# Kernel tuning notes

Hardware: AMD Instinct MI355X
Metric: run time of the kernel (lower is better)

Reference implementation:

```python
import jax, jax.numpy as jnp
import numpy as np

B, N, D, H = 2, 1024, 512, 16
DH = D // H  # d_head = 32
NEG_INF = -1e9
LN_EPS = 1e-5


def setup_inputs() -> dict:
    key = jax.random.key(0)
    ks = jax.random.split(key, 12)
    x = jax.random.normal(ks[0], (B, N, D), dtype=jnp.float32)
    pdist = jax.random.uniform(ks[1], (B, N, N), dtype=jnp.float32)
    angle = jax.random.normal(ks[2], (B, N, N, 2), dtype=jnp.float32)
    adj = jax.random.uniform(ks[3], (B, N, N), dtype=jnp.float32)
    mask = jnp.zeros((B, 1, 1, N), dtype=bool)
    # parameters
    gamma_p = jnp.ones((H,), dtype=jnp.float32)
    gamma_adj = jnp.ones((H,), dtype=jnp.float32)
    w_bias = jax.random.normal(ks[4], (H, 2), dtype=jnp.float32) / np.sqrt(2.0)   # Linear(2,H).weight
    att_w = jax.random.normal(ks[5], (3 * H * DH, D), dtype=jnp.float32) / np.sqrt(D)  # Linear(D,3HDh).weight
    ff_w = jax.random.normal(ks[6], (D, H * DH), dtype=jnp.float32) / np.sqrt(H * DH)  # Linear(HDh,D).weight
    ff_b = jnp.zeros((D,), dtype=jnp.float32)
    ln_w = jnp.ones((D,), dtype=jnp.float32)
    ln_b = jnp.zeros((D,), dtype=jnp.float32)
    return dict(x=x, pdist=pdist, angle=angle, adj=adj, mask=mask,
                gamma_p=gamma_p, gamma_adj=gamma_adj, w_bias=w_bias,
                att_w=att_w, ff_w=ff_w, ff_b=ff_b, ln_w=ln_w, ln_b=ln_b)


def reference(x, pdist, angle, adj, mask, gamma_p, gamma_adj, w_bias,
              att_w, ff_w, ff_b, ln_w, ln_b):
    bsz, n_atoms, _ = x.shape
    # QKV projection
    qkv = x @ att_w.T                              # [B,N,3*H*DH]
    wq, wk, wv = jnp.split(qkv, 3, axis=-1)
    wq = wq.reshape(bsz, n_atoms, H, DH)
    wk = wk.reshape(bsz, n_atoms, H, DH)
    wv = wv.reshape(bsz, n_atoms, H, DH)
    # scores with additive biases
    score = jnp.einsum('bihd,bjhd->bhij', wq, wk) / jnp.sqrt(jnp.float32(DH))
    score = score - gamma_p[None, :, None, None] * pdist[:, None]
    angle_bias = jnp.einsum('bijc,hc->bhij', angle, w_bias)
    score = score + angle_bias
    score = score + gamma_adj[None, :, None, None] * adj[:, None]
    score = jnp.where(mask, NEG_INF, score)
    prob = jax.nn.softmax(score, axis=-1)          # [B,H,N,N]
    att_vec = jnp.einsum('bhij,bjhd->bihd', prob, wv).reshape(bsz, n_atoms, H * DH)
    ff_out = att_vec @ ff_w.T + ff_b               # [B,N,D]
    y = x + ff_out
    mu = jnp.mean(y, axis=-1, keepdims=True)
    var = jnp.mean(jnp.square(y - mu), axis=-1, keepdims=True)
    return (y - mu) / jnp.sqrt(var + LN_EPS) * ln_w + ln_b
```

## Files before the change

kernel.cpp:

```cpp
#include <hip/hip_runtime.h>
#include <hip/hip_bf16.h>
#include <stdint.h>

#define DEVI __device__ __forceinline__

typedef __attribute__((ext_vector_type(4))) float f32x4;
typedef __attribute__((ext_vector_type(16))) float f32x16;
typedef __attribute__((ext_vector_type(8))) short bf16x8;

constexpr int nB = 2, nN = 1024, nD = 512, nH = 16, nDH = 32;

DEVI unsigned short f2bf(float x) {
  unsigned u = __float_as_uint(x);
  return (unsigned short)((u + 0x7fffu + ((u >> 16) & 1u)) >> 16);
}
DEVI float bf2f(unsigned short s) { return __uint_as_float(((unsigned)s) << 16); }
DEVI unsigned pk2(float lo, float hi_) {
  return (unsigned)f2bf(lo) | ((unsigned)f2bf(hi_) << 16);
}
DEVI float bperm(int srclane, float v) {
  return __int_as_float(__builtin_amdgcn_ds_bpermute(srclane << 2, __float_as_int(v)));
}
DEVI void gload16(const void* g, void* l) {
  __builtin_amdgcn_global_load_lds((const __attribute__((address_space(1))) void*)g,
                                   (__attribute__((address_space(3))) void*)l, 16, 0, 0);
}

__global__ __launch_bounds__(256) void cvt_kernel(const float* __restrict__ x,
                                                  const float* __restrict__ aw,
                                                  const float* __restrict__ fw,
                                                  unsigned short* __restrict__ xb,
                                                  unsigned short* __restrict__ awb,
                                                  unsigned short* __restrict__ fwb) {
  int i = blockIdx.x * 256 + threadIdx.x;
  const float* src; unsigned short* dst; int base;
  if (i < 262144)      { src = x;  dst = xb;  base = i; }
  else if (i < 458752) { src = aw; dst = awb; base = i - 262144; }
  else                 { src = fw; dst = fwb; base = i - 458752; }
  float4 v = reinterpret_cast<const float4*>(src)[base];
  ushort4 o;
  o.x = f2bf(v.x); o.y = f2bf(v.y); o.z = f2bf(v.z); o.w = f2bf(v.w);
  reinterpret_cast<ushort4*>(dst)[base] = o;
}

template <int BM, int BN, int MODE>
__global__ __launch_bounds__(256) void gemm_bt(const unsigned short* __restrict__ A,
                                               const unsigned short* __restrict__ Bw,
                                               unsigned short* __restrict__ q,
                                               unsigned short* __restrict__ kmat,
                                               unsigned short* __restrict__ vm,
                                               float* __restrict__ C,
                                               int K, int Ncols) {
  constexpr int MW = BM / 2, NW = BN / 2;
  constexpr int MF = MW / 16, NF = NW / 16;
  constexpr int IA = BM / 16, IB = BN / 16, PW = (IA + IB) / 4;
  __shared__ __align__(16) unsigned short sA[BM * 32];
  __shared__ __align__(16) unsigned short sB[BN * 32];
  const int tid = threadIdx.x, wid = tid >> 6, lane = tid & 63;
  const int wr = wid >> 1, wc = wid & 1;
  const long rowA = (long)blockIdx.x * BM;
  const long rowB = (long)blockIdx.y * BN;
  const int srow = lane >> 2, scol = (lane & 3) * 8;

  f32x4 acc[MF][NF];
#pragma unroll
  for (int mm = 0; mm < MF; ++mm)
#pragma unroll
    for (int nn = 0; nn < NF; ++nn)
#pragma unroll
      for (int r = 0; r < 4; ++r) acc[mm][nn][r] = 0.f;

  for (int k0 = 0; k0 < K; k0 += 32) {
    __syncthreads();
#pragma unroll
    for (int j = 0; j < PW; ++j) {
      int g = wid + 4 * j;
      if (g < IA) {
        gload16(&A[(rowA + g * 16 + srow) * K + k0 + scol], &sA[g * 512]);
      } else {
        int c = g - IA;
        gload16(&Bw[(rowB + c * 16 + srow) * K + k0 + scol], &sB[c * 512]);
      }
    }
    __syncthreads();
    const int kg = (lane >> 4) * 8, rlo = lane & 15;
    bf16x8 af[MF], bfv[NF];
#pragma unroll
    for (int mm = 0; mm < MF; ++mm)
      af[mm] = *reinterpret_cast<const bf16x8*>(&sA[(MW * wr + 16 * mm + rlo) * 32 + kg]);
#pragma unroll
    for (int nn = 0; nn < NF; ++nn)
      bfv[nn] = *reinterpret_cast<const bf16x8*>(&sB[(NW * wc + 16 * nn + rlo) * 32 + kg]);
#pragma unroll
    for (int mm = 0; mm < MF; ++mm)
#pragma unroll
      for (int nn = 0; nn < NF; ++nn)
        acc[mm][nn] = __builtin_amdgcn_mfma_f32_16x16x32_bf16(af[mm], bfv[nn],
                                                              acc[mm][nn], 0, 0, 0);
  }

#pragma unroll
  for (int mm = 0; mm < MF; ++mm)
#pragma unroll
    for (int nn = 0; nn < NF; ++nn)
#pragma unroll
      for (int r = 0; r < 4; ++r) {
        float v = acc[mm][nn][r];
        int row = (int)rowA + MW * wr + 16 * mm + (lane >> 4) * 4 + r;
        int col = (int)rowB + NW * wc + 16 * nn + (lane & 15);
        if constexpr (MODE == 0) {
          int s = col >> 9, rem = col & 511;
          int h = rem >> 5, d = rem & 31;
          int b = row >> 10, n = row & 1023;
          long idx = ((long)(b * nH + h) * nN + n) * nDH + d;
          if (s == 0)      q[idx]    = f2bf(v * 0.1767766952966369f);
          else if (s == 1) kmat[idx] = f2bf(v);
          else             vm[idx]   = f2bf(v);
        } else {
          C[(long)row * Ncols + col] = v;
        }
      }
}

__global__ __launch_bounds__(256) void vtrans_kernel(const unsigned short* __restrict__ vm,
                                                     unsigned short* __restrict__ vtt) {
  const int g = blockIdx.x, bh = g >> 3, oct = g & 7;
  const int t = threadIdx.x;
  __shared__ unsigned short tile[32][36];
  for (int s = 0; s < 4; ++s) {
    const int jt = oct * 4 + s;
    {
      int r = t >> 3, c4 = (t & 7) * 4;
      *reinterpret_cast<ushort4*>(&tile[r][c4]) = *reinterpret_cast<const ushort4*>(
          vm + ((long)bh * nN + jt * 32 + r) * 32 + c4);
    }
    __syncthreads();
    {
      int d = t >> 3, j4 = (t & 7) * 4;
      ushort4 o;
      o.x = tile[j4][d]; o.y = tile[j4 + 1][d];
      o.z = tile[j4 + 2][d]; o.w = tile[j4 + 3][d];
      *reinterpret_cast<ushort4*>(vtt + ((long)bh * 32 + jt) * 1024 + d * 32 + j4) = o;
    }
    __syncthreads();
  }
}

__global__ __launch_bounds__(512, 4) void attn_kernel(
    const unsigned short* __restrict__ qm, const unsigned short* __restrict__ km,
    const unsigned short* __restrict__ vtt,
    const float* __restrict__ pdist, const float* __restrict__ angle,
    const float* __restrict__ adj, const unsigned char* __restrict__ mask,
    const float* __restrict__ gamma_p, const float* __restrict__ gamma_adj,
    const float* __restrict__ w_bias,
    unsigned short* __restrict__ po, float* __restrict__ pm, float* __restrict__ pl) {
  const int b = blockIdx.x >> 5, it = blockIdx.x & 31;
  const int jc = blockIdx.y, hg = blockIdx.z;
  const int tid = threadIdx.x, wid = tid >> 6, lane = tid & 63;
  const int h = hg * 8 + wid;
  const int li = lane & 31, hi = lane >> 5;
  const int ibase = it * 32;

  __shared__ __align__(16) float s_pd[32 * 32], s_adj[32 * 32];
  __shared__ __align__(16) float s_a0[32 * 32], s_a1[32 * 32];
  __shared__ __align__(16) float s_mkf[32];

  const float gp = gamma_p[h], ga = gamma_adj[h];
  const float wb0 = w_bias[2 * h], wb1 = w_bias[2 * h + 1];

  const unsigned short* qb = qm + ((long)(b * nH + h) * nN + ibase) * nDH;
  const bf16x8 qf0 = *reinterpret_cast<const bf16x8*>(qb + li * 32 + hi * 8);
  const bf16x8 qf1 = *reinterpret_cast<const bf16x8*>(qb + li * 32 + 16 + hi * 8);

  f32x16 o;
#pragma unroll
  for (int r = 0; r < 16; ++r) o[r] = 0.f;
  float mrun = -INFINITY, lrun = 0.f;

  for (int s = 0; s < 8; ++s) {
    const int jt = jc * 8 + s, jbase = jt * 32;
    __syncthreads();
    {
      int r = (tid >> 3) & 31, c = tid & 7;
      const float* src = (tid < 256 ? pdist : adj) +
                         ((long)b * nN + ibase + r) * nN + jbase + c * 4;
      float4 v = *reinterpret_cast<const float4*>(src);
      float* dst = (tid < 256 ? s_pd : s_adj) + r * 32 + ((c ^ (r & 7)) << 2);
      *reinterpret_cast<float4*>(dst) = v;
    }
    {
      int r = tid >> 4, p = tid & 15;
      float4 v = *reinterpret_cast<const float4*>(
          angle + (((long)b * nN + ibase + r) * nN + jbase + p * 2) * 2);
      int off = r * 32 + (((p >> 1) ^ (r & 7)) << 2) + (p & 1) * 2;
      *reinterpret_cast<float2*>(s_a0 + off) = make_float2(v.x, v.z);
      *reinterpret_cast<float2*>(s_a1 + off) = make_float2(v.y, v.w);
    }
    if (tid < 32) s_mkf[tid] = mask[b * nN + jbase + tid] ? -1e9f : 0.f;
    __syncthreads();

    const unsigned short* kb = km + ((long)(b * nH + h) * nN + jbase) * nDH;
    bf16x8 kf0 = *reinterpret_cast<const bf16x8*>(kb + li * 32 + hi * 8);
    bf16x8 kf1 = *reinterpret_cast<const bf16x8*>(kb + li * 32 + 16 + hi * 8);
    f32x16 sc;
#pragma unroll
    for (int r = 0; r < 16; ++r) sc[r] = 0.f;
    sc = __builtin_amdgcn_mfma_f32_32x32x16_bf16(kf0, qf0, sc, 0, 0, 0);
    sc = __builtin_amdgcn_mfma_f32_32x32x16_bf16(kf1, qf1, sc, 0, 0, 0);

    float sv[16];
    float tmax = -INFINITY;
#pragma unroll
    for (int g = 0; g < 4; ++g) {
      const int cs = (((2 * g + hi) ^ (li & 7)) << 2);
      f32x4 pdq = *reinterpret_cast<const f32x4*>(s_pd + li * 32 + cs);
      f32x4 adq = *reinterpret_cast<const f32x4*>(s_adj + li * 32 + cs);
      f32x4 a0q = *reinterpret_cast<const f32x4*>(s_a0 + li * 32 + cs);
      f32x4 a1q = *reinterpret_cast<const f32x4*>(s_a1 + li * 32 + cs);
      f32x4 mkq = *reinterpret_cast<const f32x4*>(s_mkf + 8 * g + 4 * hi);
#pragma unroll
      for (int u = 0; u < 4; ++u) {
        float x = sc[4 * g + u] - gp * pdq[u] + wb0 * a0q[u] + wb1 * a1q[u]
                  + ga * adq[u] + mkq[u];
        sv[4 * g + u] = x;
        tmax = fmaxf(tmax, x);
      }
    }
    tmax = fmaxf(tmax, __shfl_xor(tmax, 32));
    if (__any((int)(tmax > mrun + 8.f))) {
      float mnew = fmaxf(mrun, tmax);
      float alpha = __expf(mrun - mnew);
      lrun *= alpha;
#pragma unroll
      for (int r = 0; r < 16; ++r) o[r] *= bperm((r & 3) + 8 * (r >> 2) + 4 * hi, alpha);
      mrun = mnew;
    }
    float psum = 0.f;
#pragma unroll
    for (int r = 0; r < 16; ++r) { sv[r] = __expf(sv[r] - mrun); psum += sv[r]; }
    psum += __shfl_xor(psum, 32);
    lrun += psum;

    unsigned ow[8], rw[8];
#pragma unroll
    for (int t = 0; t < 8; ++t) ow[t] = pk2(sv[2 * t], sv[2 * t + 1]);
#pragma unroll
    for (int t = 0; t < 8; ++t) rw[t] = __shfl_xor(ow[t], 32);
    union U { unsigned u[4]; bf16x8 v; };
    U u0, u1;
    if (hi == 0) {
      u0.u[0] = ow[0]; u0.u[1] = ow[1]; u0.u[2] = rw[0]; u0.u[3] = rw[1];
      u1.u[0] = ow[4]; u1.u[1] = ow[5]; u1.u[2] = rw[4]; u1.u[3] = rw[5];
    } else {
      u0.u[0] = rw[2]; u0.u[1] = rw[3]; u0.u[2] = ow[2]; u0.u[3] = ow[3];
      u1.u[0] = rw[6]; u1.u[1] = rw[7]; u1.u[2] = ow[6]; u1.u[3] = ow[7];
    }

    const unsigned short* vb = vtt + ((long)(b * nH + h) * 32 + jt) * 1024;
    bf16x8 vf0 = *reinterpret_cast<const bf16x8*>(vb + li * 32 + hi * 8);
    bf16x8 vf1 = *reinterpret_cast<const bf16x8*>(vb + li * 32 + 16 + hi * 8);
    o = __builtin_amdgcn_mfma_f32_32x32x16_bf16(u0.v, vf0, o, 0, 0, 0);
    o = __builtin_amdgcn_mfma_f32_32x32x16_bf16(u1.v, vf1, o, 0, 0, 0);
  }

  const long task = (((long)(b * nH + h) * 32 + it) * 4 + jc);
  unsigned short* pob = po + task * 1024;
#pragma unroll
  for (int r = 0; r < 16; ++r) {
    const int irow = (r & 3) + 8 * (r >> 2) + 4 * hi;
    pob[irow * 32 + li] = f2bf(o[r]);
  }
  if (hi == 0) { pm[task * 32 + li] = mrun; pl[task * 32 + li] = lrun; }
}

__global__ __launch_bounds__(256) void merge_kernel(const unsigned short* __restrict__ po,
                                                    const float* __restrict__ pm,
                                                    const float* __restrict__ pl,
                                                    unsigned short* __restrict__ attb) {
  const int x = blockIdx.x;
  const int t = threadIdx.x;
  const int i = t >> 3, d4 = (t & 7) * 4;
  const long tb = (long)x * 4;
  float m[4], l[4];
#pragma unroll
  for (int c = 0; c < 4; ++c) { m[c] = pm[(tb + c) * 32 + i]; l[c] = pl[(tb + c) * 32 + i]; }
  float M = fmaxf(fmaxf(m[0], m[1]), fmaxf(m[2], m[3]));
  float L = 0.f, w[4];
#pragma unroll
  for (int c = 0; c < 4; ++c) { w[c] = __expf(m[c] - M); L += w[c] * l[c]; }
  float o0 = 0, o1 = 0, o2 = 0, o3 = 0;
#pragma unroll
  for (int c = 0; c < 4; ++c) {
    ushort4 v = *reinterpret_cast<const ushort4*>(po + (tb + c) * 1024 + i * 32 + d4);
    o0 += w[c] * bf2f(v.x); o1 += w[c] * bf2f(v.y);
    o2 += w[c] * bf2f(v.z); o3 += w[c] * bf2f(v.w);
  }
  const float inv = 1.f / L;
  const int b = x >> 9, hh = (x >> 5) & 15, it = x & 31;
  ushort4 ov;
  ov.x = f2bf(o0 * inv); ov.y = f2bf(o1 * inv);
  ov.z = f2bf(o2 * inv); ov.w = f2bf(o3 * inv);
  *reinterpret_cast<ushort4*>(attb + ((long)b * nN + it * 32 + i) * nD + hh * 32 + d4) = ov;
}

__global__ __launch_bounds__(256) void ln_kernel(const float* __restrict__ x,
                                                 const float* __restrict__ ffc,
                                                 const float* __restrict__ ffb,
                                                 const float* __restrict__ lnw,
                                                 const float* __restrict__ lnb,
                                                 float* __restrict__ out) {
  const int row = blockIdx.x, tid = threadIdx.x;
  const int wid = tid >> 6, lane = tid & 63;
  const int c = tid * 2;
  const long base = (long)row * nD + c;
  float2 xv = *reinterpret_cast<const float2*>(x + base);
  float2 cv = *reinterpret_cast<const float2*>(ffc + base);
  float2 bv = *reinterpret_cast<const float2*>(ffb + c);
  float y0 = xv.x + cv.x + bv.x, y1 = xv.y + cv.y + bv.y;
  float s = y0 + y1, s2 = y0 * y0 + y1 * y1;
#pragma unroll
  for (int off = 1; off < 64; off <<= 1) {
    s += __shfl_xor(s, off);
    s2 += __shfl_xor(s2, off);
  }
  __shared__ float red[8];
  if (lane == 0) { red[wid] = s; red[4 + wid] = s2; }
  __syncthreads();
  s = red[0] + red[1] + red[2] + red[3];
  s2 = red[4] + red[5] + red[6] + red[7];
  const float mu = s * (1.f / nD);
  const float var = s2 * (1.f / nD) - mu * mu;
  const float rs = rsqrtf(var + 1e-5f);
  float2 wv = *reinterpret_cast<const float2*>(lnw + c);
  float2 lv = *reinterpret_cast<const float2*>(lnb + c);
  float2 ov;
  ov.x = (y0 - mu) * rs * wv.x + lv.x;
  ov.y = (y1 - mu) * rs * wv.y + lv.y;
  *reinterpret_cast<float2*>(out + base) = ov;
}

extern "C" void kernel_launch(void* const* d_in, const int* in_sizes, int n_in,
                              void* d_out, int out_size, void* d_ws, size_t ws_size,
                              hipStream_t stream) {
  const float* x         = (const float*)d_in[0];
  const float* pdist     = (const float*)d_in[1];
  const float* angle     = (const float*)d_in[2];
  const float* adj       = (const float*)d_in[3];
  const unsigned char* mask = (const unsigned char*)d_in[4];
  const float* gamma_p   = (const float*)d_in[5];
  const float* gamma_adj = (const float*)d_in[6];
  const float* w_bias    = (const float*)d_in[7];
  const float* att_w     = (const float*)d_in[8];
  const float* ff_w      = (const float*)d_in[9];
  const float* ff_b      = (const float*)d_in[10];
  const float* ln_w      = (const float*)d_in[11];
  const float* ln_b      = (const float*)d_in[12];
  float* out = (float*)d_out;

  char* ws = (char*)d_ws;
  float*          ffc  = (float*)(ws);
  unsigned short* xb   = (unsigned short*)(ws + 0x400000);
  unsigned short* vm   = (unsigned short*)(ws + 0x600000);
  unsigned short* awb  = (unsigned short*)(ws + 0x800000);
  unsigned short* fwb  = (unsigned short*)(ws + 0x980000);
  unsigned short* qm   = (unsigned short*)(ws + 0xA00000);
  unsigned short* km   = (unsigned short*)(ws + 0xC00000);
  unsigned short* vtt  = (unsigned short*)(ws + 0xE00000);
  unsigned short* po   = (unsigned short*)(ws);
  float*          pm   = (float*)(ws + 0x800000);
  float*          pl   = (float*)(ws + 0x880000);
  unsigned short* attb = km;

  hipLaunchKernelGGL(cvt_kernel, dim3(2048), dim3(256), 0, stream,
                     x, att_w, ff_w, xb, awb, fwb);
  hipLaunchKernelGGL((gemm_bt<64, 128, 0>), dim3(32, 12), dim3(256), 0, stream,
                     xb, awb, qm, km, vm, nullptr, 512, 0);
  hipLaunchKernelGGL(vtrans_kernel, dim3(256), dim3(256), 0, stream, vm, vtt);
  hipLaunchKernelGGL(attn_kernel, dim3(64, 4, 2), dim3(512), 0, stream,
                     qm, km, vtt, pdist, angle, adj, mask,
                     gamma_p, gamma_adj, w_bias, po, pm, pl);
  hipLaunchKernelGGL(merge_kernel, dim3(1024), dim3(256), 0, stream,
                     po, pm, pl, attb);
  hipLaunchKernelGGL((gemm_bt<64, 64, 1>), dim3(32, 8), dim3(256), 0, stream,
                     attb, fwb, nullptr, nullptr, nullptr, ffc, 512, 512);
  hipLaunchKernelGGL(ln_kernel, dim3(2048), dim3(256), 0, stream,
                     x, ffc, ff_b, ln_w, ln_b, out);
}
```

Measured before the change: 155.6 us.

## Double-buffer LDS in GEMM and attention; merge head groups into 1024-thread blocks

Both the projection GEMM and the attention kernel now use two LDS buffers, so the next tile's global-to-LDS loads are issued before the current tile is computed. This removes one barrier per iteration and overlaps load latency with MFMA work. The attention kernel now runs all 16 heads in one 1024-thread block instead of two 8-head blocks. That halves the redundant loading of the pdist/adj/angle tiles, and the mask is loaded once into LDS for the whole row. The cost is a doubled LDS footprint, larger blocks, and fewer total blocks, which may lower occupancy.

```diff
diff --git a/kernel.cpp b/kernel.cpp
--- a/kernel.cpp
+++ b/kernel.cpp
@@ -44,18 +44,18 @@
 }
 
 template <int BM, int BN, int MODE>
-__global__ __launch_bounds__(256) void gemm_bt(const unsigned short* __restrict__ A,
-                                               const unsigned short* __restrict__ Bw,
-                                               unsigned short* __restrict__ q,
-                                               unsigned short* __restrict__ kmat,
-                                               unsigned short* __restrict__ vm,
-                                               float* __restrict__ C,
-                                               int K, int Ncols) {
+__global__ __launch_bounds__(256, 4) void gemm_bt(const unsigned short* __restrict__ A,
+                                                  const unsigned short* __restrict__ Bw,
+                                                  unsigned short* __restrict__ q,
+                                                  unsigned short* __restrict__ kmat,
+                                                  unsigned short* __restrict__ vm,
+                                                  float* __restrict__ C,
+                                                  int K, int Ncols) {
   constexpr int MW = BM / 2, NW = BN / 2;
   constexpr int MF = MW / 16, NF = NW / 16;
   constexpr int IA = BM / 16, IB = BN / 16, PW = (IA + IB) / 4;
-  __shared__ __align__(16) unsigned short sA[BM * 32];
-  __shared__ __align__(16) unsigned short sB[BN * 32];
+  __shared__ __align__(16) unsigned short sA[2][BM * 32];
+  __shared__ __align__(16) unsigned short sB[2][BN * 32];
   const int tid = threadIdx.x, wid = tid >> 6, lane = tid & 63;
   const int wr = wid >> 1, wc = wid & 1;
   const long rowA = (long)blockIdx.x * BM;
@@ -70,33 +70,46 @@
 #pragma unroll
       for (int r = 0; r < 4; ++r) acc[mm][nn][r] = 0.f;
 
-  for (int k0 = 0; k0 < K; k0 += 32) {
-    __syncthreads();
+  auto stage = [&](int t, int pb) {
+    const int k0 = t * 32;
 #pragma unroll
     for (int j = 0; j < PW; ++j) {
       int g = wid + 4 * j;
       if (g < IA) {
-        gload16(&A[(rowA + g * 16 + srow) * K + k0 + scol], &sA[g * 512]);
+        gload16(&A[(rowA + g * 16 + srow) * K + k0 + scol], &sA[pb][g * 512]);
       } else {
         int c = g - IA;
-        gload16(&Bw[(rowB + c * 16 + srow) * K + k0 + scol], &sB[c * 512]);
+        gload16(&Bw[(rowB + c * 16 + srow) * K + k0 + scol], &sB[pb][c * 512]);
       }
     }
-    __syncthreads();
+  };
+  auto comp = [&](int pb) {
     const int kg = (lane >> 4) * 8, rlo = lane & 15;
     bf16x8 af[MF], bfv[NF];
 #pragma unroll
     for (int mm = 0; mm < MF; ++mm)
-      af[mm] = *reinterpret_cast<const bf16x8*>(&sA[(MW * wr + 16 * mm + rlo) * 32 + kg]);
+      af[mm] = *reinterpret_cast<const bf16x8*>(&sA[pb][(MW * wr + 16 * mm + rlo) * 32 + kg]);
 #pragma unroll
     for (int nn = 0; nn < NF; ++nn)
-      bfv[nn] = *reinterpret_cast<const bf16x8*>(&sB[(NW * wc + 16 * nn + rlo) * 32 + kg]);
+      bfv[nn] = *reinterpret_cast<const bf16x8*>(&sB[pb][(NW * wc + 16 * nn + rlo) * 32 + kg]);
 #pragma unroll
     for (int mm = 0; mm < MF; ++mm)
 #pragma unroll
       for (int nn = 0; nn < NF; ++nn)
         acc[mm][nn] = __builtin_amdgcn_mfma_f32_16x16x32_bf16(af[mm], bfv[nn],
                                                               acc[mm][nn], 0, 0, 0);
+  };
+
+  const int NT = K / 32;
+  stage(0, 0);
+  __syncthreads();
+  for (int t = 0; t < NT; t += 2) {
+    if (t + 1 < NT) stage(t + 1, 1);
+    comp(0);
+    __syncthreads();
+    if (t + 2 < NT) stage(t + 2, 0);
+    if (t + 1 < NT) comp(1);
+    __syncthreads();
   }
 
 #pragma unroll
@@ -146,7 +159,7 @@
   }
 }
 
-__global__ __launch_bounds__(512, 4) void attn_kernel(
+__global__ __launch_bounds__(1024, 4) void attn_kernel(
     const unsigned short* __restrict__ qm, const unsigned short* __restrict__ km,
     const unsigned short* __restrict__ vtt,
     const float* __restrict__ pdist, const float* __restrict__ angle,
@@ -155,15 +168,15 @@
     const float* __restrict__ w_bias,
     unsigned short* __restrict__ po, float* __restrict__ pm, float* __restrict__ pl) {
   const int b = blockIdx.x >> 5, it = blockIdx.x & 31;
-  const int jc = blockIdx.y, hg = blockIdx.z;
+  const int jc = blockIdx.y;
   const int tid = threadIdx.x, wid = tid >> 6, lane = tid & 63;
-  const int h = hg * 8 + wid;
+  const int h = wid;
   const int li = lane & 31, hi = lane >> 5;
   const int ibase = it * 32;
 
-  __shared__ __align__(16) float s_pd[32 * 32], s_adj[32 * 32];
-  __shared__ __align__(16) float s_a0[32 * 32], s_a1[32 * 32];
-  __shared__ __align__(16) float s_mkf[32];
+  __shared__ __align__(16) float s_pd[2][1024], s_adj[2][1024];
+  __shared__ __align__(16) float s_a0[2][1024], s_a1[2][1024];
+  __shared__ __align__(16) float s_mk[1024];
 
   const float gp = gamma_p[h], ga = gamma_adj[h];
   const float wb0 = w_bias[2 * h], wb1 = w_bias[2 * h + 1];
@@ -177,28 +190,28 @@
   for (int r = 0; r < 16; ++r) o[r] = 0.f;
   float mrun = -INFINITY, lrun = 0.f;
 
-  for (int s = 0; s < 8; ++s) {
-    const int jt = jc * 8 + s, jbase = jt * 32;
-    __syncthreads();
-    {
+  auto stage = [&](int s, int pb) {
+    const int jbase = (jc * 8 + s) * 32;
+    if (tid < 512) {
       int r = (tid >> 3) & 31, c = tid & 7;
       const float* src = (tid < 256 ? pdist : adj) +
                          ((long)b * nN + ibase + r) * nN + jbase + c * 4;
       float4 v = *reinterpret_cast<const float4*>(src);
-      float* dst = (tid < 256 ? s_pd : s_adj) + r * 32 + ((c ^ (r & 7)) << 2);
+      float* dst = (tid < 256 ? s_pd[pb] : s_adj[pb]) + r * 32 + ((c ^ (r & 7)) << 2);
       *reinterpret_cast<float4*>(dst) = v;
-    }
-    {
-      int r = tid >> 4, p = tid & 15;
+    } else {
+      int t2 = tid - 512;
+      int r = t2 >> 4, p = t2 & 15;
       float4 v = *reinterpret_cast<const float4*>(
           angle + (((long)b * nN + ibase + r) * nN + jbase + p * 2) * 2);
       int off = r * 32 + (((p >> 1) ^ (r & 7)) << 2) + (p & 1) * 2;
-      *reinterpret_cast<float2*>(s_a0 + off) = make_float2(v.x, v.z);
-      *reinterpret_cast<float2*>(s_a1 + off) = make_float2(v.y, v.w);
-    }
-    if (tid < 32) s_mkf[tid] = mask[b * nN + jbase + tid] ? -1e9f : 0.f;
-    __syncthreads();
-
+      *reinterpret_cast<float2*>(s_a0[pb] + off) = make_float2(v.x, v.z);
+      *reinterpret_cast<float2*>(s_a1[pb] + off) = make_float2(v.y, v.w);
+    }
+  };
+
+  auto comp = [&](int s, int pb) {
+    const int jt = jc * 8 + s, jbase = jt * 32;
     const unsigned short* kb = km + ((long)(b * nH + h) * nN + jbase) * nDH;
     bf16x8 kf0 = *reinterpret_cast<const bf16x8*>(kb + li * 32 + hi * 8);
     bf16x8 kf1 = *reinterpret_cast<const bf16x8*>(kb + li * 32 + 16 + hi * 8);
@@ -213,11 +226,11 @@
 #pragma unroll
     for (int g = 0; g < 4; ++g) {
       const int cs = (((2 * g + hi) ^ (li & 7)) << 2);
-      f32x4 pdq = *reinterpret_cast<const f32x4*>(s_pd + li * 32 + cs);
-      f32x4 adq = *reinterpret_cast<const f32x4*>(s_adj + li * 32 + cs);
-      f32x4 a0q = *reinterpret_cast<const f32x4*>(s_a0 + li * 32 + cs);
-      f32x4 a1q = *reinterpret_cast<const f32x4*>(s_a1 + li * 32 + cs);
-      f32x4 mkq = *reinterpret_cast<const f32x4*>(s_mkf + 8 * g + 4 * hi);
+      f32x4 pdq = *reinterpret_cast<const f32x4*>(s_pd[pb] + li * 32 + cs);
+      f32x4 adq = *reinterpret_cast<const f32x4*>(s_adj[pb] + li * 32 + cs);
+      f32x4 a0q = *reinterpret_cast<const f32x4*>(s_a0[pb] + li * 32 + cs);
+      f32x4 a1q = *reinterpret_cast<const f32x4*>(s_a1[pb] + li * 32 + cs);
+      f32x4 mkq = *reinterpret_cast<const f32x4*>(s_mk + jbase + 8 * g + 4 * hi);
 #pragma unroll
       for (int u = 0; u < 4; ++u) {
         float x = sc[4 * g + u] - gp * pdq[u] + wb0 * a0q[u] + wb1 * a1q[u]
@@ -261,6 +274,18 @@
     bf16x8 vf1 = *reinterpret_cast<const bf16x8*>(vb + li * 32 + 16 + hi * 8);
     o = __builtin_amdgcn_mfma_f32_32x32x16_bf16(u0.v, vf0, o, 0, 0, 0);
     o = __builtin_amdgcn_mfma_f32_32x32x16_bf16(u1.v, vf1, o, 0, 0, 0);
+  };
+
+  s_mk[tid] = mask[b * nN + tid] ? -1e9f : 0.f;
+  stage(0, 0);
+  __syncthreads();
+  for (int s = 0; s < 8; s += 2) {
+    if (s + 1 < 8) stage(s + 1, 1);
+    comp(s, 0);
+    __syncthreads();
+    if (s + 2 < 8) stage(s + 2, 0);
+    comp(s + 1, 1);
+    __syncthreads();
   }
 
   const long task = (((long)(b * nH + h) * 32 + it) * 4 + jc);
@@ -376,7 +401,7 @@
   hipLaunchKernelGGL((gemm_bt<64, 128, 0>), dim3(32, 12), dim3(256), 0, stream,
                      xb, awb, qm, km, vm, nullptr, 512, 0);
   hipLaunchKernelGGL(vtrans_kernel, dim3(256), dim3(256), 0, stream, vm, vtt);
-  hipLaunchKernelGGL(attn_kernel, dim3(64, 4, 2), dim3(512), 0, stream,
+  hipLaunchKernelGGL(attn_kernel, dim3(64, 4), dim3(1024), 0, stream,
                      qm, km, vtt, pdist, angle, adj, mask,
                      gamma_p, gamma_adj, w_bias, po, pm, pl);
   hipLaunchKernelGGL(merge_kernel, dim3(1024), dim3(256), 0, stream,
```

Measured after the change: 162.7 us. +4.6%, slower.
